# Optimization experiments

Measured on AMD Instinct MI355X. Metric: run time of the kernel, lower is better.

Reference implementation:

```python
import jax, jax.numpy as jnp
import numpy as np

VOCAB = 5000
HIDDEN = 512
BATCH = 64
SEQ = 256


def setup_inputs() -> dict:
    key = jax.random.key(0)
    ks = jax.random.split(key, 8)
    s = 0.02
    return {
        "X": jax.random.randint(ks[0], (BATCH, SEQ), 0, VOCAB),
        "state": jnp.zeros((1, BATCH, HIDDEN), jnp.float32),
        # PyTorch GRU params: weight_ih (3H, V), weight_hh (3H, H), biases (3H,)
        "W_ih": jax.random.normal(ks[1], (3 * HIDDEN, VOCAB), jnp.float32) * s,
        "W_hh": jax.random.normal(ks[2], (3 * HIDDEN, HIDDEN), jnp.float32) * s,
        "b_ih": jax.random.normal(ks[3], (3 * HIDDEN,), jnp.float32) * s,
        "b_hh": jax.random.normal(ks[4], (3 * HIDDEN,), jnp.float32) * s,
        # dense: Linear(hidden, vocab)
        "W_out": jax.random.normal(ks[5], (VOCAB, HIDDEN), jnp.float32) * s,
        "b_out": jax.random.normal(ks[6], (VOCAB,), jnp.float32) * s,
    }


def reference(X, state, W_ih, W_hh, b_ih, b_hh, W_out, b_out):
    V = W_ih.shape[1]
    H = W_hh.shape[1]
    # d2l.to_onehot + torch.stack -> (seq, batch, vocab), seq-first for GRU
    onehot = jax.nn.one_hot(X.T, V, dtype=W_ih.dtype)  # (S, B, V)
    # input-side GEMM for all timesteps at once (cuDNN does the same batching)
    x_proj = jnp.einsum('sbv,gv->sbg', onehot, W_ih) + b_ih  # (S, B, 3H)

    h0 = state[0]  # (B, H)

    def step(h, xp):
        gi_r, gi_z, gi_n = jnp.split(xp, 3, axis=-1)
        gh = h @ W_hh.T + b_hh
        gh_r, gh_z, gh_n = jnp.split(gh, 3, axis=-1)
        r = jax.nn.sigmoid(gi_r + gh_r)
        z = jax.nn.sigmoid(gi_z + gh_z)
        n = jnp.tanh(gi_n + r * gh_n)
        h_new = (1.0 - z) * n + z * h
        return h_new, h_new

    hT, Y = jax.lax.scan(step, h0, x_proj)  # Y: (S, B, H)
    out = Y.reshape(-1, H) @ W_out.T + b_out  # (S*B, V)
    return out, hT[None]  # state shape (1, B, H)
```

## Files before the change

### kernel.cpp

```cpp
#include <hip/hip_runtime.h>

typedef __attribute__((ext_vector_type(8))) short bf16x8;
typedef __attribute__((ext_vector_type(4))) float f32x4;
typedef __attribute__((ext_vector_type(4))) int i32x4;
typedef unsigned short ushort_t;
typedef unsigned int uint_t;

#define VOCAB 5000
#define HID   512
#define B_    64
#define SEQ_  256
#define H3    1536
#define NPAD  5120
#define NREC  32

__device__ __forceinline__ ushort_t f2bf(float f){
  uint_t u = __float_as_uint(f);
  u = u + 0x7fffu + ((u >> 16) & 1u);
  return (ushort_t)(u >> 16);
}
__device__ __forceinline__ float bf2f(ushort_t s){
  return __uint_as_float(((uint_t)s) << 16);
}

__device__ __forceinline__ uint_t agent_load_u32(const uint_t* p){
  uint_t v;
  asm volatile("global_load_dword %0, %1, off sc1\n\t"
               "s_waitcnt vmcnt(0)" : "=v"(v) : "v"(p) : "memory");
  return v;
}
__device__ __forceinline__ void agent_store_u32(uint_t* p, uint_t v){
  asm volatile("global_store_dword %0, %1, off sc1" :: "v"(p), "v"(v) : "memory");
}
__device__ __forceinline__ void agent_store_u16(ushort_t* p, ushort_t v){
  uint_t vv = v;
  asm volatile("global_store_short %0, %1, off sc1" :: "v"(p), "v"(vv) : "memory");
}

__global__ void k_transpose(const float* __restrict__ W, float* __restrict__ WT){
  __shared__ float tile[32][33];
  const int bv = blockIdx.x * 32;
  const int bg = blockIdx.y * 32;
  const int tx = threadIdx.x, ty = threadIdx.y;
  #pragma unroll
  for(int r = 0; r < 32; r += 8){
    int g = bg + ty + r, v = bv + tx;
    tile[ty + r][tx] = (v < VOCAB) ? W[(size_t)g * VOCAB + v] : 0.f;
  }
  __syncthreads();
  #pragma unroll
  for(int r = 0; r < 32; r += 8){
    int v = bv + ty + r, g = bg + tx;
    if(v < VOCAB) WT[(size_t)v * H3 + g] = tile[tx][ty + r];
  }
}

__global__ void k_cvt_wout(const float* __restrict__ W, ushort_t* __restrict__ WP){
  int idx = (blockIdx.x * 256 + threadIdx.x) * 4;
  if(idx >= NPAD * HID) return;
  float x0 = 0.f, x1 = 0.f, x2 = 0.f, x3 = 0.f;
  if(idx < VOCAB * HID){
    const float4 v = *(const float4*)(W + idx);
    x0 = v.x; x1 = v.y; x2 = v.z; x3 = v.w;
  }
  ushort4 o; o.x = f2bf(x0); o.y = f2bf(x1); o.z = f2bf(x2); o.w = f2bf(x3);
  *(ushort4*)(WP + idx) = o;
}

__global__ void k_gather(const int* __restrict__ X, const float* __restrict__ WT,
                         const float* __restrict__ bih, ushort_t* __restrict__ xp){
  const int sb = blockIdx.x;
  const int s = sb >> 6, b = sb & 63;
  const int x = X[b * SEQ_ + s];
  const float4* src = (const float4*)(WT + (size_t)x * H3);
  const float4* bi  = (const float4*)bih;
  for(int i = threadIdx.x; i < H3 / 4; i += 256){
    float4 v = src[i], c = bi[i];
    ushort4 o;
    o.x = f2bf(v.x + c.x); o.y = f2bf(v.y + c.y);
    o.z = f2bf(v.z + c.z); o.w = f2bf(v.w + c.w);
    ((ushort4*)(xp + (size_t)sb * H3))[i] = o;
  }
}

__global__ void __launch_bounds__(256, 1) k_rec(
    const float* __restrict__ Whh, const float* __restrict__ bhh,
    const float* __restrict__ state, const ushort_t* __restrict__ xp,
    ushort_t* __restrict__ hbuf,
    ushort_t* __restrict__ Y,
    float* __restrict__ hT,
    uint_t* flags)
{
  __shared__ ushort_t Wl[96][520];
  __shared__ float bl[96];
  const int g = blockIdx.x, tid = threadIdx.x;
  const int dom = g >> 4, sub = g & 15;
  const int jb = sub * 32;

  for(int idx = tid; idx < 96 * 512; idx += 256){
    int r = idx >> 9, c = idx & 511;
    int jgr = r / 48, rem = r % 48;
    int gate = rem >> 4, jl = jgr * 16 + (rem & 15);
    Wl[r][c] = f2bf(Whh[((size_t)(gate * HID + jb + jl)) * HID + c]);
  }
  if(tid < 96){
    int jgr = tid / 48, rem = tid % 48;
    int gate = rem >> 4, jl = jgr * 16 + (rem & 15);
    bl[tid] = bhh[gate * HID + jb + jl];
  }

  const int lane = tid & 63, wv = tid >> 6;
  const int l15 = lane & 15, lhi = lane >> 4;
  const int jg = wv >> 1;
  const int j  = jb + jg * 16 + l15;
  const int rbase = jg * 48;
  const int bband = dom * 32 + (wv & 1) * 16;

  float hprev[4]; int brow[4];
  #pragma unroll
  for(int i = 0; i < 4; i++){
    brow[i] = bband + lhi * 4 + i;
    hprev[i] = state[brow[i] * HID + j];
  }

  #pragma unroll
  for(int i = 0; i < 4; i++) agent_store_u16(hbuf + brow[i] * HID + j, f2bf(hprev[i]));
  asm volatile("s_waitcnt vmcnt(0)" ::: "memory");
  __syncthreads();
  if(tid == 0) agent_store_u32(flags + g * 32, 1u);

  const int fidx = dom * 16 + ((lane + sub) & 15);

  for(int t = 0; t < SEQ_; ++t){
    const ushort_t* hin  = hbuf + (t & 1) * (B_ * HID);
    ushort_t*       hout = hbuf + ((t + 1) & 1) * (B_ * HID);

    float gir[4], giz[4], gin_[4];
    const ushort_t* xr = xp + (size_t)t * B_ * H3;
    #pragma unroll
    for(int i = 0; i < 4; i++){
      const ushort_t* p = xr + (size_t)brow[i] * H3 + j;
      gir[i] = bf2f(p[0]); giz[i] = bf2f(p[HID]); gin_[i] = bf2f(p[2 * HID]);
    }

    if(lane < 16){
      const uint_t need = (uint_t)(t + 1);
      int gd = 0;
      while(agent_load_u32(flags + fidx * 32) < need){
        __builtin_amdgcn_s_sleep(1);
        if(++gd > 200000) break;
      }
    }

    i32x4 tmp[16];
    const char* abase = (const char*)(hin + (size_t)(bband + l15) * HID + 8 * lhi);
    #define LDH(i, off) asm volatile("global_load_dwordx4 %0, %1, off offset:" #off " sc1" \
                                     : "=v"(tmp[i]) : "v"(abase) : "memory");
    LDH(0,0)   LDH(1,64)   LDH(2,128)  LDH(3,192)
    LDH(4,256) LDH(5,320)  LDH(6,384)  LDH(7,448)
    LDH(8,512) LDH(9,576)  LDH(10,640) LDH(11,704)
    LDH(12,768) LDH(13,832) LDH(14,896) LDH(15,960)
    #undef LDH
    asm volatile("s_waitcnt vmcnt(0)" ::: "memory");
    __builtin_amdgcn_sched_barrier(0);

    f32x4 acc0 = {0.f,0.f,0.f,0.f}, acc1 = {0.f,0.f,0.f,0.f}, acc2 = {0.f,0.f,0.f,0.f};
    #pragma unroll
    for(int kk = 0; kk < 16; kk++){
      bf16x8 a = __builtin_bit_cast(bf16x8, tmp[kk]);
      const int kc = kk * 32 + 8 * lhi;
      bf16x8 b0 = *(const bf16x8*)&Wl[rbase + l15][kc];
      bf16x8 b1 = *(const bf16x8*)&Wl[rbase + 16 + l15][kc];
      bf16x8 b2 = *(const bf16x8*)&Wl[rbase + 32 + l15][kc];
      acc0 = __builtin_amdgcn_mfma_f32_16x16x32_bf16(a, b0, acc0, 0, 0, 0);
      acc1 = __builtin_amdgcn_mfma_f32_16x16x32_bf16(a, b1, acc1, 0, 0, 0);
      acc2 = __builtin_amdgcn_mfma_f32_16x16x32_bf16(a, b2, acc2, 0, 0, 0);
    }

    const float cr = bl[rbase + l15], cz = bl[rbase + 16 + l15], cn = bl[rbase + 32 + l15];
    float hn4[4]; ushort_t hb4[4];
    #pragma unroll
    for(int i = 0; i < 4; i++){
      float r = 1.f / (1.f + expf(-(gir[i] + acc0[i] + cr)));
      float z = 1.f / (1.f + expf(-(giz[i] + acc1[i] + cz)));
      float n = tanhf(gin_[i] + r * (acc2[i] + cn));
      hn4[i] = (1.f - z) * n + z * hprev[i];
      hprev[i] = hn4[i];
      hb4[i] = f2bf(hn4[i]);
      agent_store_u16(hout + (size_t)brow[i] * HID + j, hb4[i]);
    }
    asm volatile("s_waitcnt vmcnt(0)" ::: "memory");
    __syncthreads();
    if(tid == 0) agent_store_u32(flags + g * 32, (uint_t)(t + 2));

    #pragma unroll
    for(int i = 0; i < 4; i++){
      Y[(size_t)t * B_ * HID + (size_t)brow[i] * HID + j] = hb4[i];
      if(t == SEQ_ - 1) hT[brow[i] * HID + j] = hn4[i];
    }
  }
}

__global__ void __launch_bounds__(256) k_outgemm(
    const ushort_t* __restrict__ Y, const ushort_t* __restrict__ WP,
    const float* __restrict__ bout, float* __restrict__ out)
{
  __shared__ ushort_t At[128][40];
  __shared__ ushort_t Bt[128][40];
  const int tid = threadIdx.x;
  const int sb0 = blockIdx.x * 128, n0 = blockIdx.y * 128;
  const int lane = tid & 63, wv = tid >> 6;
  const int l15 = lane & 15, lhi = lane >> 4;
  const int wm = wv >> 1, wn = wv & 1;

  f32x4 acc[4][4];
  #pragma unroll
  for(int a = 0; a < 4; a++)
    #pragma unroll
    for(int b = 0; b < 4; b++) acc[a][b] = (f32x4){0.f,0.f,0.f,0.f};

  for(int kt = 0; kt < 16; ++kt){
    const int k0 = kt * 32;
    __syncthreads();
    #pragma unroll
    for(int hh = 0; hh < 2; ++hh){
      int idx = tid + hh * 256;
      int row = idx >> 2, seg = idx & 3;
      int4 va = *(const int4*)(Y  + (size_t)(sb0 + row) * HID + k0 + seg * 8);
      *(int4*)&At[row][seg * 8] = va;
      int4 vb = *(const int4*)(WP + (size_t)(n0 + row) * HID + k0 + seg * 8);
      *(int4*)&Bt[row][seg * 8] = vb;
    }
    __syncthreads();
    bf16x8 a[4], b[4];
    #pragma unroll
    for(int mi = 0; mi < 4; mi++) a[mi] = *(const bf16x8*)&At[wm * 64 + mi * 16 + l15][8 * lhi];
    #pragma unroll
    for(int ni = 0; ni < 4; ni++) b[ni] = *(const bf16x8*)&Bt[wn * 64 + ni * 16 + l15][8 * lhi];
    #pragma unroll
    for(int mi = 0; mi < 4; mi++)
      #pragma unroll
      for(int ni = 0; ni < 4; ni++)
        acc[mi][ni] = __builtin_amdgcn_mfma_f32_16x16x32_bf16(a[mi], b[ni], acc[mi][ni], 0, 0, 0);
  }

  #pragma unroll
  for(int mi = 0; mi < 4; mi++){
    #pragma unroll
    for(int ni = 0; ni < 4; ni++){
      int v = n0 + wn * 64 + ni * 16 + l15;
      if(v < VOCAB){
        float bb = bout[v];
        #pragma unroll
        for(int i = 0; i < 4; i++){
          int sb = sb0 + wm * 64 + mi * 16 + lhi * 4 + i;
          out[(size_t)sb * VOCAB + v] = acc[mi][ni][i] + bb;
        }
      }
    }
  }
}

extern "C" void kernel_launch(void* const* d_in, const int* in_sizes, int n_in,
                              void* d_out, int out_size, void* d_ws, size_t ws_size,
                              hipStream_t stream)
{
  const int*   X     = (const int*)  d_in[0];
  const float* state = (const float*)d_in[1];
  const float* Wih   = (const float*)d_in[2];
  const float* Whh   = (const float*)d_in[3];
  const float* bih   = (const float*)d_in[4];
  const float* bhh   = (const float*)d_in[5];
  const float* Wout  = (const float*)d_in[6];
  const float* bout  = (const float*)d_in[7];
  float* out = (float*)d_out;
  float* hT  = out + (size_t)SEQ_ * B_ * VOCAB;

  char* ws = (char*)d_ws;
  const size_t off_WihT  = 4096;
  const size_t off_WoutP = off_WihT  + (size_t)VOCAB * H3  * sizeof(float);
  const size_t off_Y     = off_WoutP + (size_t)NPAD  * HID * sizeof(ushort_t);
  const size_t off_h     = off_Y     + (size_t)SEQ_ * B_ * HID * sizeof(ushort_t);
  const size_t off_xp    = off_h     + (size_t)2 * B_ * HID * sizeof(ushort_t);

  uint_t*   flags = (uint_t*)  ws;
  float*    WihT  = (float*)   (ws + off_WihT);
  ushort_t* WoutP = (ushort_t*)(ws + off_WoutP);
  ushort_t* Ybuf  = (ushort_t*)(ws + off_Y);
  ushort_t* hbuf  = (ushort_t*)(ws + off_h);
  ushort_t* xp    = (ushort_t*)(ws + off_xp);

  (void)hipMemsetAsync(d_ws, 0, 4096, stream);
  hipLaunchKernelGGL(k_transpose, dim3(157, 48), dim3(32, 8), 0, stream, Wih, WihT);
  hipLaunchKernelGGL(k_cvt_wout, dim3((NPAD * HID / 4 + 255) / 256), dim3(256), 0, stream, Wout, WoutP);
  hipLaunchKernelGGL(k_gather, dim3(SEQ_ * B_), dim3(256), 0, stream, X, WihT, bih, xp);
  hipLaunchKernelGGL(k_rec, dim3(NREC), dim3(256), 0, stream,
                     Whh, bhh, state, xp, hbuf, Ybuf, hT, flags);
  hipLaunchKernelGGL(k_outgemm, dim3(128, 40), dim3(256), 0, stream, Ybuf, WoutP, bout, out);
}
```

Measured before the change: 1.442 ms.

## Fuse recurrence and output GEMM into one persistent kernel with flag-driven overlap

Merges the GRU recurrence kernel and the output projection GEMM into a single persistent launch. 32 blocks run the recurrence and publish per-step flags, while 224 other blocks consume each timestep's hidden states as soon as all recurrence blocks have finished it. Each consumer computes a 64x128 output tile, loading W_out directly from global memory. This hides the large output GEMM behind the serial recurrence, at the cost of smaller, less reusing GEMM tiles, extra flag polling traffic, and a dependency on all 256 blocks being co-resident.

```diff
diff --git a/kernel.cpp b/kernel.cpp
--- a/kernel.cpp
+++ b/kernel.cpp
@@ -13,6 +13,8 @@
 #define H3    1536
 #define NPAD  5120
 #define NREC  32
+#define NGEM  224
+#define NTILE (SEQ_ * 40)
 
 __device__ __forceinline__ ushort_t f2bf(float f){
   uint_t u = __float_as_uint(f);
@@ -83,180 +85,204 @@
   }
 }
 
-__global__ void __launch_bounds__(256, 1) k_rec(
+__global__ void __launch_bounds__(256, 1) k_mega(
     const float* __restrict__ Whh, const float* __restrict__ bhh,
     const float* __restrict__ state, const ushort_t* __restrict__ xp,
-    ushort_t* __restrict__ hbuf,
-    ushort_t* __restrict__ Y,
-    float* __restrict__ hT,
-    uint_t* flags)
+    const ushort_t* __restrict__ WP, const float* __restrict__ bout,
+    ushort_t* __restrict__ hbuf, ushort_t* __restrict__ Y,
+    float* __restrict__ out, float* __restrict__ hT, uint_t* flags)
 {
-  __shared__ ushort_t Wl[96][520];
-  __shared__ float bl[96];
-  const int g = blockIdx.x, tid = threadIdx.x;
-  const int dom = g >> 4, sub = g & 15;
-  const int jb = sub * 32;
-
-  for(int idx = tid; idx < 96 * 512; idx += 256){
-    int r = idx >> 9, c = idx & 511;
-    int jgr = r / 48, rem = r % 48;
-    int gate = rem >> 4, jl = jgr * 16 + (rem & 15);
-    Wl[r][c] = f2bf(Whh[((size_t)(gate * HID + jb + jl)) * HID + c]);
-  }
-  if(tid < 96){
-    int jgr = tid / 48, rem = tid % 48;
-    int gate = rem >> 4, jl = jgr * 16 + (rem & 15);
-    bl[tid] = bhh[gate * HID + jb + jl];
-  }
-
+  __shared__ __align__(16) char smem[100352];
+  const int bid = blockIdx.x, tid = threadIdx.x;
   const int lane = tid & 63, wv = tid >> 6;
   const int l15 = lane & 15, lhi = lane >> 4;
-  const int jg = wv >> 1;
-  const int j  = jb + jg * 16 + l15;
-  const int rbase = jg * 48;
-  const int bband = dom * 32 + (wv & 1) * 16;
-
-  float hprev[4]; int brow[4];
-  #pragma unroll
-  for(int i = 0; i < 4; i++){
-    brow[i] = bband + lhi * 4 + i;
-    hprev[i] = state[brow[i] * HID + j];
-  }
-
-  #pragma unroll
-  for(int i = 0; i < 4; i++) agent_store_u16(hbuf + brow[i] * HID + j, f2bf(hprev[i]));
-  asm volatile("s_waitcnt vmcnt(0)" ::: "memory");
-  __syncthreads();
-  if(tid == 0) agent_store_u32(flags + g * 32, 1u);
-
-  const int fidx = dom * 16 + ((lane + sub) & 15);
-
-  for(int t = 0; t < SEQ_; ++t){
-    const ushort_t* hin  = hbuf + (t & 1) * (B_ * HID);
-    ushort_t*       hout = hbuf + ((t + 1) & 1) * (B_ * HID);
-
-    float gir[4], giz[4], gin_[4];
-    const ushort_t* xr = xp + (size_t)t * B_ * H3;
+
+  if(bid < NREC){
+    ushort_t (*Wl)[520] = (ushort_t(*)[520])smem;
+    float* bl = (float*)(smem + 96 * 520 * 2);
+    const int g = bid;
+    const int dom = g >> 4, sub = g & 15;
+    const int jb = sub * 32;
+
+    for(int idx = tid; idx < 96 * 512; idx += 256){
+      int r = idx >> 9, c = idx & 511;
+      int jgr = r / 48, rem = r % 48;
+      int gate = rem >> 4, jl = jgr * 16 + (rem & 15);
+      Wl[r][c] = f2bf(Whh[((size_t)(gate * HID + jb + jl)) * HID + c]);
+    }
+    if(tid < 96){
+      int jgr = tid / 48, rem = tid % 48;
+      int gate = rem >> 4, jl = jgr * 16 + (rem & 15);
+      bl[tid] = bhh[gate * HID + jb + jl];
+    }
+
+    const int jg = wv >> 1;
+    const int j  = jb + jg * 16 + l15;
+    const int rbase = jg * 48;
+    const int bband = dom * 32 + (wv & 1) * 16;
+
+    float hprev[4]; int brow[4];
     #pragma unroll
     for(int i = 0; i < 4; i++){
-      const ushort_t* p = xr + (size_t)brow[i] * H3 + j;
-      gir[i] = bf2f(p[0]); giz[i] = bf2f(p[HID]); gin_[i] = bf2f(p[2 * HID]);
-    }
-
-    if(lane < 16){
-      const uint_t need = (uint_t)(t + 1);
-      int gd = 0;
-      while(agent_load_u32(flags + fidx * 32) < need){
-        __builtin_amdgcn_s_sleep(1);
-        if(++gd > 200000) break;
-      }
-    }
-
-    i32x4 tmp[16];
-    const char* abase = (const char*)(hin + (size_t)(bband + l15) * HID + 8 * lhi);
-    #define LDH(i, off) asm volatile("global_load_dwordx4 %0, %1, off offset:" #off " sc1" \
-                                     : "=v"(tmp[i]) : "v"(abase) : "memory");
-    LDH(0,0)   LDH(1,64)   LDH(2,128)  LDH(3,192)
-    LDH(4,256) LDH(5,320)  LDH(6,384)  LDH(7,448)
-    LDH(8,512) LDH(9,576)  LDH(10,640) LDH(11,704)
-    LDH(12,768) LDH(13,832) LDH(14,896) LDH(15,960)
-    #undef LDH
-    asm volatile("s_waitcnt vmcnt(0)" ::: "memory");
-    __builtin_amdgcn_sched_barrier(0);
-
-    f32x4 acc0 = {0.f,0.f,0.f,0.f}, acc1 = {0.f,0.f,0.f,0.f}, acc2 = {0.f,0.f,0.f,0.f};
+      brow[i] = bband + lhi * 4 + i;
+      hprev[i] = state[brow[i] * HID + j];
+    }
+
     #pragma unroll
-    for(int kk = 0; kk < 16; kk++){
-      bf16x8 a = __builtin_bit_cast(bf16x8, tmp[kk]);
-      const int kc = kk * 32 + 8 * lhi;
-      bf16x8 b0 = *(const bf16x8*)&Wl[rbase + l15][kc];
-      bf16x8 b1 = *(const bf16x8*)&Wl[rbase + 16 + l15][kc];
-      bf16x8 b2 = *(const bf16x8*)&Wl[rbase + 32 + l15][kc];
-      acc0 = __builtin_amdgcn_mfma_f32_16x16x32_bf16(a, b0, acc0, 0, 0, 0);
-      acc1 = __builtin_amdgcn_mfma_f32_16x16x32_bf16(a, b1, acc1, 0, 0, 0);
-      acc2 = __builtin_amdgcn_mfma_f32_16x16x32_bf16(a, b2, acc2, 0, 0, 0);
-    }
-
-    const float cr = bl[rbase + l15], cz = bl[rbase + 16 + l15], cn = bl[rbase + 32 + l15];
-    float hn4[4]; ushort_t hb4[4];
-    #pragma unroll
-    for(int i = 0; i < 4; i++){
-      float r = 1.f / (1.f + expf(-(gir[i] + acc0[i] + cr)));
-      float z = 1.f / (1.f + expf(-(giz[i] + acc1[i] + cz)));
-      float n = tanhf(gin_[i] + r * (acc2[i] + cn));
-      hn4[i] = (1.f - z) * n + z * hprev[i];
-      hprev[i] = hn4[i];
-      hb4[i] = f2bf(hn4[i]);
-      agent_store_u16(hout + (size_t)brow[i] * HID + j, hb4[i]);
-    }
+    for(int i = 0; i < 4; i++) agent_store_u16(hbuf + brow[i] * HID + j, f2bf(hprev[i]));
     asm volatile("s_waitcnt vmcnt(0)" ::: "memory");
     __syncthreads();
-    if(tid == 0) agent_store_u32(flags + g * 32, (uint_t)(t + 2));
-
-    #pragma unroll
-    for(int i = 0; i < 4; i++){
-      Y[(size_t)t * B_ * HID + (size_t)brow[i] * HID + j] = hb4[i];
-      if(t == SEQ_ - 1) hT[brow[i] * HID + j] = hn4[i];
-    }
-  }
-}
-
-__global__ void __launch_bounds__(256) k_outgemm(
-    const ushort_t* __restrict__ Y, const ushort_t* __restrict__ WP,
-    const float* __restrict__ bout, float* __restrict__ out)
-{
-  __shared__ ushort_t At[128][40];
-  __shared__ ushort_t Bt[128][40];
-  const int tid = threadIdx.x;
-  const int sb0 = blockIdx.x * 128, n0 = blockIdx.y * 128;
-  const int lane = tid & 63, wv = tid >> 6;
-  const int l15 = lane & 15, lhi = lane >> 4;
-  const int wm = wv >> 1, wn = wv & 1;
-
-  f32x4 acc[4][4];
-  #pragma unroll
-  for(int a = 0; a < 4; a++)
-    #pragma unroll
-    for(int b = 0; b < 4; b++) acc[a][b] = (f32x4){0.f,0.f,0.f,0.f};
-
-  for(int kt = 0; kt < 16; ++kt){
-    const int k0 = kt * 32;
-    __syncthreads();
-    #pragma unroll
-    for(int hh = 0; hh < 2; ++hh){
-      int idx = tid + hh * 256;
-      int row = idx >> 2, seg = idx & 3;
-      int4 va = *(const int4*)(Y  + (size_t)(sb0 + row) * HID + k0 + seg * 8);
-      *(int4*)&At[row][seg * 8] = va;
-      int4 vb = *(const int4*)(WP + (size_t)(n0 + row) * HID + k0 + seg * 8);
-      *(int4*)&Bt[row][seg * 8] = vb;
-    }
-    __syncthreads();
-    bf16x8 a[4], b[4];
-    #pragma unroll
-    for(int mi = 0; mi < 4; mi++) a[mi] = *(const bf16x8*)&At[wm * 64 + mi * 16 + l15][8 * lhi];
-    #pragma unroll
-    for(int ni = 0; ni < 4; ni++) b[ni] = *(const bf16x8*)&Bt[wn * 64 + ni * 16 + l15][8 * lhi];
-    #pragma unroll
-    for(int mi = 0; mi < 4; mi++)
-      #pragma unroll
-      for(int ni = 0; ni < 4; ni++)
-        acc[mi][ni] = __builtin_amdgcn_mfma_f32_16x16x32_bf16(a[mi], b[ni], acc[mi][ni], 0, 0, 0);
-  }
-
-  #pragma unroll
-  for(int mi = 0; mi < 4; mi++){
-    #pragma unroll
-    for(int ni = 0; ni < 4; ni++){
-      int v = n0 + wn * 64 + ni * 16 + l15;
-      if(v < VOCAB){
-        float bb = bout[v];
+    if(tid == 0) agent_store_u32(flags + g * 32, 1u);
+
+    const int fidx = dom * 16 + ((lane + sub) & 15);
+
+    for(int t = 0; t < SEQ_; ++t){
+      const ushort_t* hin  = hbuf + (t & 1) * (B_ * HID);
+      ushort_t*       hout = hbuf + ((t + 1) & 1) * (B_ * HID);
+
+      float gir[4], giz[4], gin_[4];
+      const ushort_t* xr = xp + (size_t)t * B_ * H3;
+      #pragma unroll
+      for(int i = 0; i < 4; i++){
+        const ushort_t* p = xr + (size_t)brow[i] * H3 + j;
+        gir[i] = bf2f(p[0]); giz[i] = bf2f(p[HID]); gin_[i] = bf2f(p[2 * HID]);
+      }
+
+      if(lane < 16){
+        const uint_t need = (uint_t)(t + 1);
+        int gd = 0;
+        while(agent_load_u32(flags + fidx * 32) < need){
+          __builtin_amdgcn_s_sleep(1);
+          if(++gd > 200000) break;
+        }
+      }
+
+      i32x4 tmp[16];
+      const char* abase = (const char*)(hin + (size_t)(bband + l15) * HID + 8 * lhi);
+      #define LDH(i, off) asm volatile("global_load_dwordx4 %0, %1, off offset:" #off " sc1" \
+                                       : "=v"(tmp[i]) : "v"(abase) : "memory");
+      LDH(0,0)   LDH(1,64)   LDH(2,128)  LDH(3,192)
+      LDH(4,256) LDH(5,320)  LDH(6,384)  LDH(7,448)
+      LDH(8,512) LDH(9,576)  LDH(10,640) LDH(11,704)
+      LDH(12,768) LDH(13,832) LDH(14,896) LDH(15,960)
+      #undef LDH
+      asm volatile("s_waitcnt vmcnt(0)" ::: "memory");
+      __builtin_amdgcn_sched_barrier(0);
+
+      f32x4 acc0 = {0.f,0.f,0.f,0.f}, acc1 = {0.f,0.f,0.f,0.f}, acc2 = {0.f,0.f,0.f,0.f};
+      #pragma unroll
+      for(int kk = 0; kk < 16; kk++){
+        bf16x8 a = __builtin_bit_cast(bf16x8, tmp[kk]);
+        const int kc = kk * 32 + 8 * lhi;
+        bf16x8 b0 = *(const bf16x8*)&Wl[rbase + l15][kc];
+        bf16x8 b1 = *(const bf16x8*)&Wl[rbase + 16 + l15][kc];
+        bf16x8 b2 = *(const bf16x8*)&Wl[rbase + 32 + l15][kc];
+        acc0 = __builtin_amdgcn_mfma_f32_16x16x32_bf16(a, b0, acc0, 0, 0, 0);
+        acc1 = __builtin_amdgcn_mfma_f32_16x16x32_bf16(a, b1, acc1, 0, 0, 0);
+        acc2 = __builtin_amdgcn_mfma_f32_16x16x32_bf16(a, b2, acc2, 0, 0, 0);
+      }
+
+      const float cr = bl[rbase + l15], cz = bl[rbase + 16 + l15], cn = bl[rbase + 32 + l15];
+      float hn4[4];
+      #pragma unroll
+      for(int i = 0; i < 4; i++){
+        float r = 1.f / (1.f + expf(-(gir[i] + acc0[i] + cr)));
+        float z = 1.f / (1.f + expf(-(giz[i] + acc1[i] + cz)));
+        float n = tanhf(gin_[i] + r * (acc2[i] + cn));
+        hn4[i] = (1.f - z) * n + z * hprev[i];
+        hprev[i] = hn4[i];
+        ushort_t hb = f2bf(hn4[i]);
+        agent_store_u16(hout + (size_t)brow[i] * HID + j, hb);
+        agent_store_u16(Y + (size_t)t * B_ * HID + (size_t)brow[i] * HID + j, hb);
+      }
+      asm volatile("s_waitcnt vmcnt(0)" ::: "memory");
+      __syncthreads();
+      if(tid == 0) agent_store_u32(flags + g * 32, (uint_t)(t + 2));
+
+      if(t == SEQ_ - 1){
         #pragma unroll
-        for(int i = 0; i < 4; i++){
-          int sb = sb0 + wm * 64 + mi * 16 + lhi * 4 + i;
-          out[(size_t)sb * VOCAB + v] = acc[mi][ni][i] + bb;
+        for(int i = 0; i < 4; i++) hT[brow[i] * HID + j] = hn4[i];
+      }
+    }
+  } else {
+    ushort_t (*At)[520] = (ushort_t(*)[520])smem;
+    const int gb = bid - NREC;
+
+    for(int tile = gb; tile < NTILE; tile += NGEM){
+      const int t = tile / 40, n0 = (tile % 40) * 128;
+
+      if(wv == 0){
+        const uint_t need = (uint_t)(t + 2);
+        int gd = 0;
+        while(true){
+          uint_t v = 0xffffffffu;
+          if(lane < 32) v = agent_load_u32(flags + lane * 32);
+          if(__all(v >= need)) break;
+          __builtin_amdgcn_s_sleep(64);
+          if(++gd > 2000000) break;
         }
       }
+      __syncthreads();
+
+      {
+        const int row = tid >> 2, q = tid & 3;
+        const char* src = (const char*)(Y + (size_t)t * B_ * HID) + row * 1024 + q * 256;
+        i32x4 tv[16];
+        #define LDA(i, off) asm volatile("global_load_dwordx4 %0, %1, off offset:" #off " sc1" \
+                                         : "=v"(tv[i]) : "v"(src) : "memory");
+        LDA(0,0)   LDA(1,16)  LDA(2,32)  LDA(3,48)
+        LDA(4,64)  LDA(5,80)  LDA(6,96)  LDA(7,112)
+        LDA(8,128) LDA(9,144) LDA(10,160) LDA(11,176)
+        LDA(12,192) LDA(13,208) LDA(14,224) LDA(15,240)
+        #undef LDA
+        asm volatile("s_waitcnt vmcnt(0)" ::: "memory");
+        __builtin_amdgcn_sched_barrier(0);
+        #pragma unroll
+        for(int i = 0; i < 16; i++) *(i32x4*)&At[row][q * 128 + i * 8] = tv[i];
+      }
+      __syncthreads();
+
+      f32x4 acc[4][2];
+      #pragma unroll
+      for(int a = 0; a < 4; a++){ acc[a][0] = (f32x4){0,0,0,0}; acc[a][1] = (f32x4){0,0,0,0}; }
+
+      const ushort_t* B0 = WP + (size_t)(n0 + wv * 32 + l15) * HID;
+      const ushort_t* B1 = WP + (size_t)(n0 + wv * 32 + 16 + l15) * HID;
+      #pragma unroll
+      for(int kt = 0; kt < 16; kt++){
+        const int kc = kt * 32 + 8 * lhi;
+        bf16x8 b0 = *(const bf16x8*)(B0 + kc);
+        bf16x8 b1 = *(const bf16x8*)(B1 + kc);
+        bf16x8 a0 = *(const bf16x8*)&At[0 * 16 + l15][kc];
+        bf16x8 a1 = *(const bf16x8*)&At[1 * 16 + l15][kc];
+        bf16x8 a2 = *(const bf16x8*)&At[2 * 16 + l15][kc];
+        bf16x8 a3 = *(const bf16x8*)&At[3 * 16 + l15][kc];
+        acc[0][0] = __builtin_amdgcn_mfma_f32_16x16x32_bf16(a0, b0, acc[0][0], 0, 0, 0);
+        acc[0][1] = __builtin_amdgcn_mfma_f32_16x16x32_bf16(a0, b1, acc[0][1], 0, 0, 0);
+        acc[1][0] = __builtin_amdgcn_mfma_f32_16x16x32_bf16(a1, b0, acc[1][0], 0, 0, 0);
+        acc[1][1] = __builtin_amdgcn_mfma_f32_16x16x32_bf16(a1, b1, acc[1][1], 0, 0, 0);
+        acc[2][0] = __builtin_amdgcn_mfma_f32_16x16x32_bf16(a2, b0, acc[2][0], 0, 0, 0);
+        acc[2][1] = __builtin_amdgcn_mfma_f32_16x16x32_bf16(a2, b1, acc[2][1], 0, 0, 0);
+        acc[3][0] = __builtin_amdgcn_mfma_f32_16x16x32_bf16(a3, b0, acc[3][0], 0, 0, 0);
+        acc[3][1] = __builtin_amdgcn_mfma_f32_16x16x32_bf16(a3, b1, acc[3][1], 0, 0, 0);
+      }
+
+      #pragma unroll
+      for(int mi = 0; mi < 4; mi++){
+        #pragma unroll
+        for(int ni = 0; ni < 2; ni++){
+          const int v = n0 + wv * 32 + ni * 16 + l15;
+          if(v < VOCAB){
+            const float bb = bout[v];
+            #pragma unroll
+            for(int i = 0; i < 4; i++){
+              const int sb = t * 64 + mi * 16 + lhi * 4 + i;
+              out[(size_t)sb * VOCAB + v] = acc[mi][ni][i] + bb;
+            }
+          }
+        }
+      }
+      __syncthreads();
     }
   }
 }
@@ -294,7 +320,6 @@
   hipLaunchKernelGGL(k_transpose, dim3(157, 48), dim3(32, 8), 0, stream, Wih, WihT);
   hipLaunchKernelGGL(k_cvt_wout, dim3((NPAD * HID / 4 + 255) / 256), dim3(256), 0, stream, Wout, WoutP);
   hipLaunchKernelGGL(k_gather, dim3(SEQ_ * B_), dim3(256), 0, stream, X, WihT, bih, xp);
-  hipLaunchKernelGGL(k_rec, dim3(NREC), dim3(256), 0, stream,
-                     Whh, bhh, state, xp, hbuf, Ybuf, hT, flags);
-  hipLaunchKernelGGL(k_outgemm, dim3(128, 40), dim3(256), 0, stream, Ybuf, WoutP, bout, out);
-}
+  hipLaunchKernelGGL(k_mega, dim3(NREC + NGEM), dim3(256), 0, stream,
+                     Whh, bhh, state, xp, WoutP, bout, hbuf, Ybuf, out, hT, flags);
+}
```

Measured after the change: 1.381 ms. 1.04x faster.
